# Kernel optimization log

Measured on AMD Instinct MI355X. Metric: run time of the kernel, lower is better.

Reference implementation:

```python
import jax, jax.numpy as jnp
import numpy as np

L, K, D, V, S, B = 2, 4, 1024, 32000, 1024, 2

# Constant neighbor influence from the 2x2 grid (success_rate==0.5 for fresh blocks)
_pos = np.array([[0, 0], [0, 1], [1, 0], [1, 1]], dtype=np.float64)
_dist = np.sqrt(((_pos[:, None, :] - _pos[None, :, :]) ** 2).sum(-1))
_infl = np.where(np.eye(K, dtype=bool), 0.0, 0.5 / (1.0 + _dist)).sum(-1)
NEIGHBOR_SIG = jnp.asarray(1.0 / (1.0 + np.exp(-_infl)), dtype=jnp.float32)  # [K]


def _ln(x, g, b, eps=1e-5):
    mu = x.mean(-1, keepdims=True)
    var = ((x - mu) ** 2).mean(-1, keepdims=True)
    return (x - mu) / jnp.sqrt(var + eps) * g + b


def setup_inputs() -> dict:
    key = jax.random.key(0)
    ks = jax.random.split(key, 10)
    def n(k, shape, s):
        return jax.random.normal(k, shape, jnp.float32) * s
    return {
        "input_ids": jax.random.randint(ks[0], (B, S), 0, V),
        "embedding": n(ks[1], (V, D), 0.02),
        "pos_enc": n(ks[2], (S, D), 0.02),
        "torsion_field": jnp.zeros((D,), jnp.float32),
        "ln1_g": jnp.ones((L, D), jnp.float32),
        "ln1_b": jnp.zeros((L, D), jnp.float32),
        "base_W": n(ks[3], (L, D, D), 0.02),
        "blk_W1": n(ks[4], (L, K, D // 2, D), 0.02),
        "blk_W2": n(ks[5], (L, K, D, D // 2), 0.02),
        "blk_gate": n(ks[6], (L, K, D), 0.01),
        "prop_W": n(ks[7], (L, K, K), 0.5),
        "prop_b": jnp.zeros((L, K), jnp.float32),
        "ln2_g": jnp.ones((L, D), jnp.float32),
        "ln2_b": jnp.zeros((L, D), jnp.float32),
        "out_ln_g": jnp.ones((D,), jnp.float32),
        "out_ln_b": jnp.zeros((D,), jnp.float32),
        "lm_head_W": n(ks[8], (V, D), 0.02),
    }


def reference(input_ids, embedding, pos_enc, torsion_field, ln1_g, ln1_b,
              base_W, blk_W1, blk_W2, blk_gate, prop_W, prop_b,
              ln2_g, ln2_b, out_ln_g, out_ln_b, lm_head_W):
    h = embedding[input_ids] + pos_enc[None]  # [B,S,D]
    s = jnp.full((K,), 0.5, h.dtype)  # fresh blocks: success_rate = 0.5
    for l in range(L):
        # excitement (detached in torch via .item())
        exc0 = jax.nn.sigmoid(prop_W[l] @ s + prop_b[l])
        exc = jax.lax.stop_gradient(0.6 * exc0 + 0.4 * NEIGHBOR_SIG)  # [K]
        hn = _ln(h, ln1_g[l], ln1_b[l])
        base = hn @ base_W[l].T  # [B,S,D]
        # all K blocks are always loaded (min_blocks == max_blocks == 4)
        t = jnp.einsum('bsd,khd->bksh', hn, blk_W1[l])
        t = jax.nn.gelu(t, approximate=False)
        t = jnp.einsum('bksh,kdh->bksd', t, blk_W2[l])
        gate = jax.nn.sigmoid(blk_gate[l] + torsion_field)  # [K,D]
        t = t * gate[None, :, None, :]
        combined = jnp.einsum('bksd,k->bsd', t, exc) / exc.sum()
        h = h + (base + combined) * 0.3
        h = _ln(h, ln2_g[l], ln2_b[l])
    h = _ln(h, out_ln_g, out_ln_b)
    return h @ lm_head_W.T  # [B,S,V]
```

## Files before the change

kernel.cpp:

```cpp
#include <hip/hip_runtime.h>
#include <math.h>

typedef unsigned short u16;
typedef short s16x8 __attribute__((ext_vector_type(8)));
typedef float f32x4 __attribute__((ext_vector_type(4)));
typedef u16 u16x4 __attribute__((ext_vector_type(4)));

#define D 1024
#define MM 2048
#define HH 512
#define VV 32000

static __device__ __forceinline__ u16 f2bf(float f) {
    union { float f; unsigned int i; } c; c.f = f;
    unsigned int x = c.i;
    return (u16)((x + 0x7fffu + ((x >> 16) & 1u)) >> 16);
}
static __device__ __forceinline__ float sigm(float x) { return 1.0f / (1.0f + expf(-x)); }

static __device__ __forceinline__ void load_lds16(const u16* g, u16* l) {
    __builtin_amdgcn_global_load_lds(
        (const __attribute__((address_space(1))) unsigned int*)g,
        (__attribute__((address_space(3))) unsigned int*)l, 16, 0, 0);
}

__global__ __launch_bounds__(256) void cvt_kernel(const float* __restrict__ in,
                                                  u16* __restrict__ out, const int n4)
{
    for (int i = blockIdx.x * 256 + threadIdx.x; i < n4; i += gridDim.x * 256) {
        f32x4 v = __builtin_nontemporal_load((const f32x4*)in + i);
        u16x4 o;
#pragma unroll
        for (int j = 0; j < 4; j++) o[j] = f2bf(v[j]);
        ((u16x4*)out)[i] = o;
    }
}

__global__ __launch_bounds__(256) void cvtcat_kernel(const float* __restrict__ baseW,
    const float* __restrict__ W1, u16* __restrict__ out)
{
    const int N4 = 3072 * 1024 / 4, B4 = 1024 * 1024 / 4;
    for (int i = blockIdx.x * 256 + threadIdx.x; i < N4; i += gridDim.x * 256) {
        f32x4 v = (i < B4) ? __builtin_nontemporal_load((const f32x4*)baseW + i)
                           : __builtin_nontemporal_load((const f32x4*)W1 + (i - B4));
        u16x4 o;
#pragma unroll
        for (int j = 0; j < 4; j++) o[j] = f2bf(v[j]);
        ((u16x4*)out)[i] = o;
    }
}

__global__ __launch_bounds__(256) void embed_ln_kernel(const int* __restrict__ ids,
    const float* __restrict__ emb, const float* __restrict__ pos,
    const float* __restrict__ g, const float* __restrict__ b,
    float* __restrict__ h, u16* __restrict__ hn)
{
    const int m = blockIdx.x;
    const int s = m & 1023;
    const long id = ids[m];
    const int d = threadIdx.x * 4;
    f32x4 ev = *(const f32x4*)&emb[id * D + d];
    f32x4 pv = *(const f32x4*)&pos[(long)s * D + d];
    f32x4 x;
#pragma unroll
    for (int i = 0; i < 4; i++) x[i] = ev[i] + pv[i];
    *(f32x4*)&h[(long)m * D + d] = x;

    float sm = x[0] + x[1] + x[2] + x[3];
    float ss = x[0]*x[0] + x[1]*x[1] + x[2]*x[2] + x[3]*x[3];
#pragma unroll
    for (int off = 32; off; off >>= 1) { sm += __shfl_xor(sm, off); ss += __shfl_xor(ss, off); }
    __shared__ float red[8];
    const int wid = threadIdx.x >> 6;
    if ((threadIdx.x & 63) == 0) { red[wid] = sm; red[4 + wid] = ss; }
    __syncthreads();
    sm = red[0] + red[1] + red[2] + red[3];
    ss = red[4] + red[5] + red[6] + red[7];
    const float mu = sm * (1.0f / D);
    const float rstd = rsqrtf(ss * (1.0f / D) - mu * mu + 1e-5f);
    f32x4 gv = *(const f32x4*)&g[d];
    f32x4 bv = *(const f32x4*)&b[d];
    u16x4 o;
#pragma unroll
    for (int i = 0; i < 4; i++) o[i] = f2bf((x[i] - mu) * rstd * gv[i] + bv[i]);
    *(u16x4*)&hn[(long)m * D + d] = o;
}

__global__ __launch_bounds__(256) void resln2_kernel(float* __restrict__ h,
    const float* __restrict__ c, const float* __restrict__ g2, const float* __restrict__ b2,
    const float* __restrict__ gn, const float* __restrict__ bn_, u16* __restrict__ hn)
{
    const int row = blockIdx.x;
    const int d = threadIdx.x * 4;
    f32x4 x = *(const f32x4*)&h[(long)row * D + d];
    f32x4 cv = *(const f32x4*)&c[(long)row * D + d];
#pragma unroll
    for (int i = 0; i < 4; i++) x[i] += 0.3f * cv[i];
    float sm = x[0] + x[1] + x[2] + x[3];
    float ss = x[0]*x[0] + x[1]*x[1] + x[2]*x[2] + x[3]*x[3];
#pragma unroll
    for (int off = 32; off; off >>= 1) { sm += __shfl_xor(sm, off); ss += __shfl_xor(ss, off); }
    __shared__ float red[8];
    const int wid = threadIdx.x >> 6;
    if ((threadIdx.x & 63) == 0) { red[wid] = sm; red[4 + wid] = ss; }
    __syncthreads();
    sm = red[0] + red[1] + red[2] + red[3];
    ss = red[4] + red[5] + red[6] + red[7];
    float mu = sm * (1.0f / D);
    float rstd = rsqrtf(ss * (1.0f / D) - mu * mu + 1e-5f);
    f32x4 g2v = *(const f32x4*)&g2[d];
    f32x4 b2v = *(const f32x4*)&b2[d];
    f32x4 y;
#pragma unroll
    for (int i = 0; i < 4; i++) y[i] = (x[i] - mu) * rstd * g2v[i] + b2v[i];
    *(f32x4*)&h[(long)row * D + d] = y;

    sm = y[0] + y[1] + y[2] + y[3];
    ss = y[0]*y[0] + y[1]*y[1] + y[2]*y[2] + y[3]*y[3];
#pragma unroll
    for (int off = 32; off; off >>= 1) { sm += __shfl_xor(sm, off); ss += __shfl_xor(ss, off); }
    __syncthreads();
    if ((threadIdx.x & 63) == 0) { red[wid] = sm; red[4 + wid] = ss; }
    __syncthreads();
    sm = red[0] + red[1] + red[2] + red[3];
    ss = red[4] + red[5] + red[6] + red[7];
    mu = sm * (1.0f / D);
    rstd = rsqrtf(ss * (1.0f / D) - mu * mu + 1e-5f);
    f32x4 gnv = *(const f32x4*)&gn[d];
    f32x4 bnv = *(const f32x4*)&bn_[d];
    u16x4 o;
#pragma unroll
    for (int i = 0; i < 4; i++) o[i] = f2bf((y[i] - mu) * rstd * gnv[i] + bnv[i]);
    *(u16x4*)&hn[(long)row * D + d] = o;
}

__global__ __launch_bounds__(256) void scale_w2x_kernel(
    const float* __restrict__ W2l, const float* __restrict__ gatel,
    const float* __restrict__ tors, const float* __restrict__ pW,
    const float* __restrict__ pb, u16* __restrict__ W2eff)
{
    const float NS = 1.0f / (1.0f + expf(-0.70710678118654752f));
    float e[4], sum = 0.0f;
#pragma unroll
    for (int k = 0; k < 4; k++) {
        float a = pb[k] + 0.5f * (pW[k*4] + pW[k*4+1] + pW[k*4+2] + pW[k*4+3]);
        e[k] = 0.6f * sigm(a) + 0.4f * NS;
        sum += e[k];
    }
    const int n = blockIdx.x >> 1;
    const int half = blockIdx.x & 1;
    const int kh = half * 1024 + threadIdx.x * 4;
    const int k = kh >> 9;
    const int hh = kh & 511;
    const float f = sigm(gatel[k * D + n] + tors[n]) * (e[k] / sum);
    f32x4 w = __builtin_nontemporal_load((const f32x4*)&W2l[((long)k * D + n) * HH + hh]);
    u16x4 o;
#pragma unroll
    for (int i = 0; i < 4; i++) o[i] = f2bf(w[i] * f);
    *(u16x4*)&W2eff[(long)n * 2048 + kh] = o;
}

template<int EPI>
__global__ __launch_bounds__(256) void gemm_t(
    const u16* __restrict__ A, const u16* __restrict__ W,
    float* __restrict__ Cf, u16* __restrict__ Cb,
    const int Kloop, const int ldk, const long ldc)
{
    if (EPI == 4) { A += blockIdx.z * 512; W += blockIdx.z * 512; }

    const int gx = gridDim.x;
    const int nwg = gx * gridDim.y;
    int lin = blockIdx.y * gx + blockIdx.x;
    lin = (lin & 7) * (nwg >> 3) + (lin >> 3);
    const int bm = (lin % gx) * 128;
    const int bn = (lin / gx) * 128;

    __shared__ __align__(16) u16 AB[8192];

    const int tid = threadIdx.x, lane = tid & 63, w = tid >> 6;
    const int wm = w >> 1, wn = w & 1;
    const int l15 = lane & 15, lk8 = (lane >> 4) * 8;

    const u16* src[4];
    u16* dst[4];
#pragma unroll
    for (int ci = 0; ci < 4; ++ci) {
        const int c = w + ci * 4;
        src[ci] = (c < 8 ? A + (long)(bm + c * 16 + l15) * ldk
                         : W + (long)(bn + (c - 8) * 16 + l15) * ldk) + lk8;
        dst[ci] = AB + c * 512;
    }

    f32x4 acc[4][4];
#pragma unroll
    for (int i = 0; i < 4; ++i)
#pragma unroll
        for (int j = 0; j < 4; ++j) acc[i][j] = f32x4{0.f, 0.f, 0.f, 0.f};

    for (int k0 = 0; k0 < Kloop; k0 += 32) {
        __syncthreads();
#pragma unroll
        for (int ci = 0; ci < 4; ++ci) load_lds16(src[ci] + k0, dst[ci]);
        __syncthreads();
        s16x8 a[4], b[4];
#pragma unroll
        for (int i = 0; i < 4; ++i) a[i] = *(const s16x8*)(AB + (wm * 4 + i) * 512 + lane * 8);
#pragma unroll
        for (int j = 0; j < 4; ++j) b[j] = *(const s16x8*)(AB + (8 + wn * 4 + j) * 512 + lane * 8);
#pragma unroll
        for (int i = 0; i < 4; ++i)
#pragma unroll
            for (int j = 0; j < 4; ++j)
                acc[i][j] = __builtin_amdgcn_mfma_f32_16x16x32_bf16(a[i], b[j], acc[i][j], 0, 0, 0);
    }

    const int r0 = (lane >> 4) * 4;
#pragma unroll
    for (int i = 0; i < 4; ++i) {
#pragma unroll
        for (int j = 0; j < 4; ++j) {
            const int n = bn + wn * 64 + j * 16 + l15;
#pragma unroll
            for (int rr = 0; rr < 4; ++rr) {
                const int m = bm + wm * 64 + i * 16 + r0 + rr;
                const float v = acc[i][j][rr];
                if (EPI == 3) {
                    if (n < 1024) {
                        Cf[(long)m * 1024 + n] = v;
                    } else {
                        const float gel = 0.5f * v * (1.0f + erff(v * 0.70710678118654752f));
                        Cb[(long)m * 2048 + (n - 1024)] = f2bf(gel);
                    }
                } else {
                    atomicAdd(&Cf[(long)m * ldc + n], v);
                }
            }
        }
    }
}

#define AU16  16384
#define HALFU 8192
#define BB0   32768

__global__ __launch_bounds__(512, 2) void gemm256_kernel(
    const u16* __restrict__ Ag, const u16* __restrict__ Wg, float* __restrict__ C)
{
    __shared__ __align__(16) u16 lds[65536];

    const int nwg = gridDim.x * gridDim.y;
    int lin = blockIdx.y * gridDim.x + blockIdx.x;
    lin = (lin & 7) * (nwg >> 3) + (lin >> 3);
    const int bm = (lin & 7) * 256;
    const int bn = (lin >> 3) * 256;

    const int tid = threadIdx.x;
    const int lane = tid & 63;
    const int w = tid >> 6;
    const int wm = w >> 2;
    const int wn = w & 3;

    const u16* aSrc = Ag + (long)(bm + w * 16 + (lane & 15)) * 1024 + ((lane >> 4) * 8);
    const u16* bSrc = Wg + (long)(bn + w * 16 + (lane & 15)) * 1024 + ((lane >> 4) * 8);
    u16* aDst = lds + w * 1024;
    u16* bDst = lds + BB0 + w * 1024;

    auto stageA = [&](int kt, int b, int kk) {
        const long co = (long)kt * 64 + kk * 32;
        load_lds16(aSrc + co,               aDst + b * AU16 + kk * 512);
        load_lds16(aSrc + co + 128 * 1024L, aDst + b * AU16 + HALFU + kk * 512);
    };
    auto stageB = [&](int kt, int b, int kk) {
        const long co = (long)kt * 64 + kk * 32;
        load_lds16(bSrc + co,               bDst + b * AU16 + kk * 512);
        load_lds16(bSrc + co + 128 * 1024L, bDst + b * AU16 + HALFU + kk * 512);
    };

    const u16* aRd = lds + wm * HALFU + lane * 8;
    const u16* bRd = lds + BB0 + (wn >> 1) * HALFU + (wn & 1) * 4096 + lane * 8;

    f32x4 acc[8][4];
#pragma unroll
    for (int i = 0; i < 8; ++i)
#pragma unroll
        for (int j = 0; j < 4; ++j) acc[i][j] = f32x4{0.f, 0.f, 0.f, 0.f};

    s16x8 F0[12], F1[12];

    stageA(0, 0, 0); stageB(0, 0, 0);
    stageA(0, 0, 1); stageB(0, 0, 1);
    stageA(1, 1, 0); stageB(1, 1, 0);
    asm volatile("s_waitcnt vmcnt(4)" ::: "memory");
    __builtin_amdgcn_s_barrier();
    __builtin_amdgcn_sched_barrier(0);

#pragma unroll
    for (int i = 0; i < 8; ++i) F0[i] = *(const s16x8*)(aRd + i * 1024);
#pragma unroll
    for (int j = 0; j < 4; ++j) F0[8 + j] = *(const s16x8*)(bRd + j * 1024);

    auto phase = [&](int p, s16x8 (&fu)[12], s16x8 (&fl)[12]) {
        const int pr = p + 1;
        const int Tr = (pr >> 1) & 15, kkr = pr & 1, br = Tr & 1;
        const u16* aR = aRd + br * AU16 + kkr * 512;
        const u16* bR = bRd + br * AU16 + kkr * 512;
#pragma unroll
        for (int i = 0; i < 8; ++i) fl[i] = *(const s16x8*)(aR + i * 1024);
#pragma unroll
        for (int j = 0; j < 4; ++j) fl[8 + j] = *(const s16x8*)(bR + j * 1024);
        const int us = 6 + 2 * p;
        const int Ts = (us >> 2) & 15, kks = (us >> 1) & 1, bs = Ts & 1;
        stageA(Ts, bs, kks);
        stageB(Ts, bs, kks);
        __builtin_amdgcn_sched_barrier(0);
        __builtin_amdgcn_s_setprio(1);
#pragma unroll
        for (int j = 0; j < 4; ++j)
#pragma unroll
            for (int i = 0; i < 8; ++i)
                acc[i][j] = __builtin_amdgcn_mfma_f32_16x16x32_bf16(fu[i], fu[8 + j], acc[i][j], 0, 0, 0);
        __builtin_amdgcn_s_setprio(0);
        __builtin_amdgcn_sched_barrier(0);
        asm volatile("s_waitcnt vmcnt(4)" ::: "memory");
        __builtin_amdgcn_s_barrier();
        __builtin_amdgcn_sched_barrier(0);
    };

    for (int p = 0; p < 32; p += 2) {
        phase(p,     F0, F1);
        phase(p + 1, F1, F0);
    }

    asm volatile("s_waitcnt vmcnt(0)" ::: "memory");
    __builtin_amdgcn_s_barrier();

    float* tp = (float*)lds + w * 1104;
    const int cl = lane & 15;
    const int r0 = (lane >> 4) * 4;
    const int rowRd = lane >> 4;
    for (int i = 0; i < 8; ++i) {
#pragma unroll
        for (int j = 0; j < 4; ++j)
#pragma unroll
            for (int rr = 0; rr < 4; ++rr)
                tp[(r0 + rr) * 68 + j * 16 + cl] = acc[i][j][rr];
#pragma unroll
        for (int rep = 0; rep < 4; ++rep) {
            const int r = rowRd + rep * 4;
            f32x4 v = *(const f32x4*)&tp[r * 68 + 4 * cl];
            *(f32x4*)&C[(long)(bm + wm * 128 + i * 16 + r) * VV + bn + wn * 64 + 4 * cl] = v;
        }
    }
}

extern "C" void kernel_launch(void* const* d_in, const int* in_sizes, int n_in,
                              void* d_out, int out_size, void* d_ws, size_t ws_size,
                              hipStream_t stream)
{
    (void)in_sizes; (void)n_in; (void)out_size; (void)ws_size;
    const int*   ids   = (const int*)d_in[0];
    const float* emb   = (const float*)d_in[1];
    const float* pos   = (const float*)d_in[2];
    const float* tors  = (const float*)d_in[3];
    const float* ln1g  = (const float*)d_in[4];
    const float* ln1b  = (const float*)d_in[5];
    const float* baseW = (const float*)d_in[6];
    const float* W1    = (const float*)d_in[7];
    const float* W2    = (const float*)d_in[8];
    const float* gate  = (const float*)d_in[9];
    const float* propW = (const float*)d_in[10];
    const float* propb = (const float*)d_in[11];
    const float* ln2g  = (const float*)d_in[12];
    const float* ln2b  = (const float*)d_in[13];
    const float* outg  = (const float*)d_in[14];
    const float* outb  = (const float*)d_in[15];
    const float* lmW   = (const float*)d_in[16];

    char* ws = (char*)d_ws;
    float* h     = (float*)(ws);
    u16*   hn    = (u16*)  (ws + (8l  << 20));
    u16*   Wcat  = (u16*)  (ws + (12l << 20));
    float* C     = (float*)(ws + (18l << 20));
    u16*   t     = (u16*)  (ws + (26l << 20));
    u16*   W2eff = (u16*)  (ws + (34l << 20));
    u16*   lmWbf = (u16*)  (ws + (12l << 20));

    embed_ln_kernel<<<MM, 256, 0, stream>>>(ids, emb, pos, ln1g, ln1b, h, hn);

    for (int l = 0; l < 2; l++) {
        cvtcat_kernel<<<1024, 256, 0, stream>>>(
            baseW + (long)l * D * D, W1 + (long)l * 4 * HH * D, Wcat);
        scale_w2x_kernel<<<2048, 256, 0, stream>>>(
            W2 + (long)l * 4 * D * HH, gate + (long)l * 4 * D, tors,
            propW + l * 16, propb + l * 4, W2eff);
        gemm_t<3><<<dim3(16, 24), 256, 0, stream>>>(hn, Wcat, C, t, 1024, 1024, 0);
        gemm_t<4><<<dim3(16, 8, 4), 256, 0, stream>>>(t, W2eff, C, nullptr, 512, 2048, 1024);
        resln2_kernel<<<MM, 256, 0, stream>>>(
            h, C, ln2g + (long)l * D, ln2b + (long)l * D,
            l == 0 ? ln1g + D : outg, l == 0 ? ln1b + D : outb, hn);
    }

    cvt_kernel<<<2048, 256, 0, stream>>>(lmW, lmWbf, VV * D / 4);
    gemm256_kernel<<<dim3(8, 125), 512, 0, stream>>>(hn, lmWbf, (float*)d_out);
}
```

Measured before the change: 418.6 us.

## Fuse base projection into second GEMM via concatenated activations and weights

Previously the first GEMM computed the base projection and the W1 up-projection together, and a split-K second GEMM used atomicAdd to accumulate the W2 products into C. Now the first GEMM computes only the GELU'd W1 output, writing it into columns 1024..3071 of a wide [2048x3072] activation buffer. A single second GEMM then multiplies that buffer by a concatenated [baseW | scaled W2] weight, giving base+combined without atomics and with one plain store. The lm-head epilogue also drops its LDS-transposed vector stores in favour of direct scalar stores, which removes a barrier but may give less coalesced output writes.

```diff
diff --git a/kernel.cpp b/kernel.cpp
--- a/kernel.cpp
+++ b/kernel.cpp
@@ -10,6 +10,7 @@
 #define MM 2048
 #define HH 512
 #define VV 32000
+#define LDA 3072
 
 static __device__ __forceinline__ u16 f2bf(float f) {
     union { float f; unsigned int i; } c; c.f = f;
@@ -36,17 +37,40 @@
     }
 }
 
-__global__ __launch_bounds__(256) void cvtcat_kernel(const float* __restrict__ baseW,
-    const float* __restrict__ W1, u16* __restrict__ out)
-{
-    const int N4 = 3072 * 1024 / 4, B4 = 1024 * 1024 / 4;
-    for (int i = blockIdx.x * 256 + threadIdx.x; i < N4; i += gridDim.x * 256) {
-        f32x4 v = (i < B4) ? __builtin_nontemporal_load((const f32x4*)baseW + i)
-                           : __builtin_nontemporal_load((const f32x4*)W1 + (i - B4));
+__global__ __launch_bounds__(256) void build_wcat2_kernel(
+    const float* __restrict__ baseWl, const float* __restrict__ W2l,
+    const float* __restrict__ gatel, const float* __restrict__ tors,
+    const float* __restrict__ pW, const float* __restrict__ pb,
+    u16* __restrict__ out)
+{
+    const float NS = 1.0f / (1.0f + expf(-0.70710678118654752f));
+    float e[4], sum = 0.0f;
+#pragma unroll
+    for (int k = 0; k < 4; k++) {
+        float a = pb[k] + 0.5f * (pW[k*4] + pW[k*4+1] + pW[k*4+2] + pW[k*4+3]);
+        e[k] = 0.6f * sigm(a) + 0.4f * NS;
+        sum += e[k];
+    }
+    const int n = blockIdx.x;
+    const int tid = threadIdx.x;
+#pragma unroll
+    for (int jj = 0; jj < 3; ++jj) {
+        const int col = jj * 1024 + tid * 4;
+        f32x4 v;
+        if (col < 1024) {
+            v = __builtin_nontemporal_load((const f32x4*)&baseWl[(long)n * 1024 + col]);
+        } else {
+            const int c2 = col - 1024;
+            const int k = c2 >> 9, hh = c2 & 511;
+            const float f = sigm(gatel[k * D + n] + tors[n]) * (e[k] / sum);
+            v = __builtin_nontemporal_load((const f32x4*)&W2l[((long)(k << 10) + n) * HH + hh]);
+#pragma unroll
+            for (int i = 0; i < 4; i++) v[i] *= f;
+        }
         u16x4 o;
 #pragma unroll
-        for (int j = 0; j < 4; j++) o[j] = f2bf(v[j]);
-        ((u16x4*)out)[i] = o;
+        for (int i = 0; i < 4; i++) o[i] = f2bf(v[i]);
+        *(u16x4*)&out[(long)n * LDA + col] = o;
     }
 }
 
@@ -83,7 +107,7 @@
     u16x4 o;
 #pragma unroll
     for (int i = 0; i < 4; i++) o[i] = f2bf((x[i] - mu) * rstd * gv[i] + bv[i]);
-    *(u16x4*)&hn[(long)m * D + d] = o;
+    *(u16x4*)&hn[(long)m * LDA + d] = o;
 }
 
 __global__ __launch_bounds__(256) void resln2_kernel(float* __restrict__ h,
@@ -131,86 +155,61 @@
     u16x4 o;
 #pragma unroll
     for (int i = 0; i < 4; i++) o[i] = f2bf((y[i] - mu) * rstd * gnv[i] + bnv[i]);
-    *(u16x4*)&hn[(long)row * D + d] = o;
-}
-
-__global__ __launch_bounds__(256) void scale_w2x_kernel(
-    const float* __restrict__ W2l, const float* __restrict__ gatel,
-    const float* __restrict__ tors, const float* __restrict__ pW,
-    const float* __restrict__ pb, u16* __restrict__ W2eff)
-{
-    const float NS = 1.0f / (1.0f + expf(-0.70710678118654752f));
-    float e[4], sum = 0.0f;
-#pragma unroll
-    for (int k = 0; k < 4; k++) {
-        float a = pb[k] + 0.5f * (pW[k*4] + pW[k*4+1] + pW[k*4+2] + pW[k*4+3]);
-        e[k] = 0.6f * sigm(a) + 0.4f * NS;
-        sum += e[k];
-    }
-    const int n = blockIdx.x >> 1;
-    const int half = blockIdx.x & 1;
-    const int kh = half * 1024 + threadIdx.x * 4;
-    const int k = kh >> 9;
-    const int hh = kh & 511;
-    const float f = sigm(gatel[k * D + n] + tors[n]) * (e[k] / sum);
-    f32x4 w = __builtin_nontemporal_load((const f32x4*)&W2l[((long)k * D + n) * HH + hh]);
-    u16x4 o;
-#pragma unroll
-    for (int i = 0; i < 4; i++) o[i] = f2bf(w[i] * f);
-    *(u16x4*)&W2eff[(long)n * 2048 + kh] = o;
-}
-
-template<int EPI>
+    *(u16x4*)&hn[(long)row * LDA + d] = o;
+}
+
+template<int EPI, int BN>
 __global__ __launch_bounds__(256) void gemm_t(
     const u16* __restrict__ A, const u16* __restrict__ W,
     float* __restrict__ Cf, u16* __restrict__ Cb,
-    const int Kloop, const int ldk, const long ldc)
-{
-    if (EPI == 4) { A += blockIdx.z * 512; W += blockIdx.z * 512; }
-
+    const int Kloop, const int ldkA, const int ldkW, const long ldc)
+{
     const int gx = gridDim.x;
     const int nwg = gx * gridDim.y;
     int lin = blockIdx.y * gx + blockIdx.x;
     lin = (lin & 7) * (nwg >> 3) + (lin >> 3);
     const int bm = (lin % gx) * 128;
-    const int bn = (lin / gx) * 128;
-
-    __shared__ __align__(16) u16 AB[8192];
+    const int bn = (lin / gx) * BN;
+
+    constexpr int NCH = 8 + BN / 16;
+    constexpr int NIT = NCH / 4;
+    __shared__ __align__(16) u16 AB[NCH * 512];
 
     const int tid = threadIdx.x, lane = tid & 63, w = tid >> 6;
     const int wm = w >> 1, wn = w & 1;
     const int l15 = lane & 15, lk8 = (lane >> 4) * 8;
 
-    const u16* src[4];
-    u16* dst[4];
-#pragma unroll
-    for (int ci = 0; ci < 4; ++ci) {
+    const u16* src[NIT];
+    u16* dst[NIT];
+#pragma unroll
+    for (int ci = 0; ci < NIT; ++ci) {
         const int c = w + ci * 4;
-        src[ci] = (c < 8 ? A + (long)(bm + c * 16 + l15) * ldk
-                         : W + (long)(bn + (c - 8) * 16 + l15) * ldk) + lk8;
+        src[ci] = (c < 8 ? A + (long)(bm + c * 16 + l15) * ldkA
+                         : W + (long)(bn + (c - 8) * 16 + l15) * ldkW) + lk8;
         dst[ci] = AB + c * 512;
     }
 
-    f32x4 acc[4][4];
+    f32x4 acc[4][BN / 32];
 #pragma unroll
     for (int i = 0; i < 4; ++i)
 #pragma unroll
-        for (int j = 0; j < 4; ++j) acc[i][j] = f32x4{0.f, 0.f, 0.f, 0.f};
+        for (int j = 0; j < BN / 32; ++j) acc[i][j] = f32x4{0.f, 0.f, 0.f, 0.f};
 
     for (int k0 = 0; k0 < Kloop; k0 += 32) {
         __syncthreads();
 #pragma unroll
-        for (int ci = 0; ci < 4; ++ci) load_lds16(src[ci] + k0, dst[ci]);
+        for (int ci = 0; ci < NIT; ++ci) load_lds16(src[ci] + k0, dst[ci]);
         __syncthreads();
-        s16x8 a[4], b[4];
+        s16x8 a[4], b[BN / 32];
 #pragma unroll
         for (int i = 0; i < 4; ++i) a[i] = *(const s16x8*)(AB + (wm * 4 + i) * 512 + lane * 8);
 #pragma unroll
-        for (int j = 0; j < 4; ++j) b[j] = *(const s16x8*)(AB + (8 + wn * 4 + j) * 512 + lane * 8);
+        for (int j = 0; j < BN / 32; ++j)
+            b[j] = *(const s16x8*)(AB + (8 + wn * (BN / 32) + j) * 512 + lane * 8);
 #pragma unroll
         for (int i = 0; i < 4; ++i)
 #pragma unroll
-            for (int j = 0; j < 4; ++j)
+            for (int j = 0; j < BN / 32; ++j)
                 acc[i][j] = __builtin_amdgcn_mfma_f32_16x16x32_bf16(a[i], b[j], acc[i][j], 0, 0, 0);
     }
 
@@ -218,21 +217,17 @@
 #pragma unroll
     for (int i = 0; i < 4; ++i) {
 #pragma unroll
-        for (int j = 0; j < 4; ++j) {
-            const int n = bn + wn * 64 + j * 16 + l15;
+        for (int j = 0; j < BN / 32; ++j) {
+            const int n = bn + wn * (BN / 2) + j * 16 + l15;
 #pragma unroll
             for (int rr = 0; rr < 4; ++rr) {
                 const int m = bm + wm * 64 + i * 16 + r0 + rr;
                 const float v = acc[i][j][rr];
-                if (EPI == 3) {
-                    if (n < 1024) {
-                        Cf[(long)m * 1024 + n] = v;
-                    } else {
-                        const float gel = 0.5f * v * (1.0f + erff(v * 0.70710678118654752f));
-                        Cb[(long)m * 2048 + (n - 1024)] = f2bf(gel);
-                    }
+                if (EPI == 0) {
+                    Cf[(long)m * ldc + n] = v;
                 } else {
-                    atomicAdd(&Cf[(long)m * ldc + n], v);
+                    const float gel = 0.5f * v * (1.0f + erff(v * 0.70710678118654752f));
+                    Cb[(long)m * ldc + n] = f2bf(gel);
                 }
             }
         }
@@ -244,7 +239,8 @@
 #define BB0   32768
 
 __global__ __launch_bounds__(512, 2) void gemm256_kernel(
-    const u16* __restrict__ Ag, const u16* __restrict__ Wg, float* __restrict__ C)
+    const u16* __restrict__ Ag, const u16* __restrict__ Wg, float* __restrict__ C,
+    const int ldkA)
 {
     __shared__ __align__(16) u16 lds[65536];
 
@@ -260,15 +256,16 @@
     const int wm = w >> 2;
     const int wn = w & 3;
 
-    const u16* aSrc = Ag + (long)(bm + w * 16 + (lane & 15)) * 1024 + ((lane >> 4) * 8);
+    const u16* aSrc = Ag + (long)(bm + w * 16 + (lane & 15)) * ldkA + ((lane >> 4) * 8);
     const u16* bSrc = Wg + (long)(bn + w * 16 + (lane & 15)) * 1024 + ((lane >> 4) * 8);
     u16* aDst = lds + w * 1024;
     u16* bDst = lds + BB0 + w * 1024;
+    const long aHalf = (long)128 * ldkA;
 
     auto stageA = [&](int kt, int b, int kk) {
         const long co = (long)kt * 64 + kk * 32;
-        load_lds16(aSrc + co,               aDst + b * AU16 + kk * 512);
-        load_lds16(aSrc + co + 128 * 1024L, aDst + b * AU16 + HALFU + kk * 512);
+        load_lds16(aSrc + co,         aDst + b * AU16 + kk * 512);
+        load_lds16(aSrc + co + aHalf, aDst + b * AU16 + HALFU + kk * 512);
     };
     auto stageB = [&](int kt, int b, int kk) {
         const long co = (long)kt * 64 + kk * 32;
@@ -332,25 +329,19 @@
     }
 
     asm volatile("s_waitcnt vmcnt(0)" ::: "memory");
-    __builtin_amdgcn_s_barrier();
-
-    float* tp = (float*)lds + w * 1104;
+
+    const int r0 = (lane >> 4) * 4;
     const int cl = lane & 15;
-    const int r0 = (lane >> 4) * 4;
-    const int rowRd = lane >> 4;
-    for (int i = 0; i < 8; ++i) {
-#pragma unroll
-        for (int j = 0; j < 4; ++j)
+#pragma unroll
+    for (int i = 0; i < 8; ++i)
+#pragma unroll
+        for (int j = 0; j < 4; ++j) {
+            const long m = bm + wm * 128 + i * 16 + r0;
+            const int n = bn + wn * 64 + j * 16 + cl;
 #pragma unroll
             for (int rr = 0; rr < 4; ++rr)
-                tp[(r0 + rr) * 68 + j * 16 + cl] = acc[i][j][rr];
-#pragma unroll
-        for (int rep = 0; rep < 4; ++rep) {
-            const int r = rowRd + rep * 4;
-            f32x4 v = *(const f32x4*)&tp[r * 68 + 4 * cl];
-            *(f32x4*)&C[(long)(bm + wm * 128 + i * 16 + r) * VV + bn + wn * 64 + 4 * cl] = v;
+                C[(m + rr) * (long)VV + n] = acc[i][j][rr];
         }
-    }
 }
 
 extern "C" void kernel_launch(void* const* d_in, const int* in_sizes, int n_in,
@@ -378,28 +369,28 @@
 
     char* ws = (char*)d_ws;
     float* h     = (float*)(ws);
-    u16*   hn    = (u16*)  (ws + (8l  << 20));
-    u16*   Wcat  = (u16*)  (ws + (12l << 20));
-    float* C     = (float*)(ws + (18l << 20));
-    u16*   t     = (u16*)  (ws + (26l << 20));
-    u16*   W2eff = (u16*)  (ws + (34l << 20));
-    u16*   lmWbf = (u16*)  (ws + (12l << 20));
-
-    embed_ln_kernel<<<MM, 256, 0, stream>>>(ids, emb, pos, ln1g, ln1b, h, hn);
+    u16*   Acat  = (u16*)  (ws + (8l  << 20));
+    float* C     = (float*)(ws + (20l << 20));
+    u16*   W1bf  = (u16*)  (ws + (28l << 20));
+    u16*   Wcat2 = (u16*)  (ws + (32l << 20));
+    u16*   lmWbf = (u16*)  (ws + (20l << 20));
+
+    embed_ln_kernel<<<MM, 256, 0, stream>>>(ids, emb, pos, ln1g, ln1b, h, Acat);
 
     for (int l = 0; l < 2; l++) {
-        cvtcat_kernel<<<1024, 256, 0, stream>>>(
-            baseW + (long)l * D * D, W1 + (long)l * 4 * HH * D, Wcat);
-        scale_w2x_kernel<<<2048, 256, 0, stream>>>(
-            W2 + (long)l * 4 * D * HH, gate + (long)l * 4 * D, tors,
-            propW + l * 16, propb + l * 4, W2eff);
-        gemm_t<3><<<dim3(16, 24), 256, 0, stream>>>(hn, Wcat, C, t, 1024, 1024, 0);
-        gemm_t<4><<<dim3(16, 8, 4), 256, 0, stream>>>(t, W2eff, C, nullptr, 512, 2048, 1024);
+        cvt_kernel<<<1024, 256, 0, stream>>>(W1 + (long)l * 4 * HH * D, W1bf, 4 * HH * D / 4);
+        build_wcat2_kernel<<<1024, 256, 0, stream>>>(
+            baseW + (long)l * D * D, W2 + (long)l * 4 * D * HH,
+            gate + (long)l * 4 * D, tors, propW + l * 16, propb + l * 4, Wcat2);
+        gemm_t<1, 128><<<dim3(16, 16), 256, 0, stream>>>(
+            Acat, W1bf, nullptr, Acat + 1024, 1024, LDA, 1024, LDA);
+        gemm_t<0, 64><<<dim3(16, 16), 256, 0, stream>>>(
+            Acat, Wcat2, C, nullptr, LDA, LDA, LDA, D);
         resln2_kernel<<<MM, 256, 0, stream>>>(
             h, C, ln2g + (long)l * D, ln2b + (long)l * D,
-            l == 0 ? ln1g + D : outg, l == 0 ? ln1b + D : outb, hn);
+            l == 0 ? ln1g + D : outg, l == 0 ? ln1b + D : outb, Acat);
     }
 
     cvt_kernel<<<2048, 256, 0, stream>>>(lmW, lmWbf, VV * D / 4);
-    gemm256_kernel<<<dim3(8, 125), 512, 0, stream>>>(hn, lmWbf, (float*)d_out);
-}
+    gemm256_kernel<<<dim3(8, 125), 512, 0, stream>>>(Acat, lmWbf, (float*)d_out, LDA);
+}
```

Measured after the change: 469.2 us. 1.12x slower.
